# Optimization experiments

Hardware: AMD Instinct MI355X
Metric: run time of the kernel (lower is better)

## Reference

```python
import jax, jax.numpy as jnp
import numpy as np

B, T, H, E, L, C = 32, 512, 512, 256, 64, 128  # batch, seq, hidden, chan_emb, latent, num_channels
IN = E + H + L  # recurrent_input_size


def setup_inputs() -> dict:
    key = jax.random.key(0)
    ks = jax.random.split(key, 8)
    marks = jax.random.randint(ks[0], (B, T), 0, C)
    # strictly increasing event times per sequence
    timestamps = jnp.cumsum(jax.random.uniform(ks[1], (B, T)), axis=1)
    latent_state = jax.random.normal(ks[2], (B, L), dtype=jnp.float32)
    emb_table = jax.random.normal(ks[3], (C, E), dtype=jnp.float32) * 0.02
    W_cell = jax.random.normal(ks[4], (IN, 7 * H), dtype=jnp.float32) * (1.0 / np.sqrt(IN))
    b_cell = jnp.zeros((7 * H,), dtype=jnp.float32)
    W_init = jax.random.normal(ks[5], (L, 6 * H), dtype=jnp.float32) * (1.0 / np.sqrt(L))
    b_init = jnp.zeros((6 * H,), dtype=jnp.float32)
    return dict(marks=marks, timestamps=timestamps, latent_state=latent_state,
                emb_table=emb_table, W_cell=W_cell, b_cell=b_cell,
                W_init=W_init, b_init=b_init)


def reference(marks, timestamps, latent_state, emb_table, W_cell, b_cell, W_init, b_init):
    # time_embedding(timestamps): inter-event durations, [B, T, 1]
    time_deltas = jnp.concatenate(
        [timestamps[:, :1], timestamps[:, 1:] - timestamps[:, :-1]], axis=1)[..., None]
    emb = emb_table[marks]                                        # [B, T, E]
    lat = jnp.broadcast_to(latent_state[:, None, :], (B, T, L))   # [B, T, L]
    recurrent_input = jnp.concatenate([emb, lat], axis=-1)        # [B, T, E+L]

    # get_init_states via init_hidden_state_network
    init = latent_state @ W_init + b_init                         # [B, 6H]
    h_d0, c_d0, c_bar0, c0, delta0, o0 = jnp.split(init, 6, axis=-1)
    h_d0, c_d0, c_bar0, c0 = (jnp.tanh(h_d0), jnp.tanh(c_d0), jnp.tanh(c_bar0), jnp.tanh(c0))
    delta0 = jax.nn.softplus(delta0)
    o0 = jax.nn.sigmoid(o0)
    state0 = jnp.concatenate([h_d0, o0, c_bar0, c0, delta0], axis=-1)  # [B, 5H]

    def step(carry, xs):
        h_d, c_d, c_bar = carry
        r, dt = xs                                   # [B, E+L], [B, 1]
        feed = jnp.concatenate([r, h_d], axis=1)     # [B, IN]
        gates = feed @ W_cell + b_cell               # [B, 7H]
        gi, gf, gz, go, gib, gfb, gd = jnp.split(gates, 7, axis=-1)
        gi, gf, go = jax.nn.sigmoid(gi), jax.nn.sigmoid(gf), jax.nn.sigmoid(go)
        gib, gfb = jax.nn.sigmoid(gib), jax.nn.sigmoid(gfb)
        gz = jnp.tanh(gz)
        gd = jax.nn.softplus(gd)
        c_t = gf * c_d + gi * gz                     # recurrence uses decayed c as c_{t-1}
        c_bar_t = gfb * c_bar + gib * gz
        c_d_t = c_bar_t + (c_t - c_bar_t) * jnp.exp(-gd * dt)
        h_d_t = go * jnp.tanh(c_d_t)
        out = jnp.concatenate([h_d_t, go, c_bar_t, c_t, gd], axis=-1)  # [B, 5H]
        return (h_d_t, c_d_t, c_bar_t), out

    xs = (jnp.moveaxis(recurrent_input, 1, 0), jnp.moveaxis(time_deltas, 1, 0))
    _, outs = jax.lax.scan(step, (h_d0, c_d0, c_bar0), xs)           # [T, B, 5H]
    hidden_states = jnp.concatenate([state0[:, None, :], jnp.moveaxis(outs, 0, 1)], axis=1)
    return hidden_states  # [B, T+1, 5H]
```

## Files before the change

kernel.cpp:

```cpp
#include <hip/hip_runtime.h>
#include <hip/hip_bf16.h>

namespace {

constexpr int kB = 32;
constexpr int kT = 512;
constexpr int kH = 512;
constexpr int kE = 256;
constexpr int kL = 64;
constexpr int kNC = 7 * kH;
constexpr int kOutRow = 5 * kH;
constexpr int kBH = kB * kH;

typedef float f32x4 __attribute__((ext_vector_type(4)));
typedef short s16x8 __attribute__((ext_vector_type(8)));
typedef __bf16 bf16x8 __attribute__((ext_vector_type(8)));
typedef unsigned int u32x4 __attribute__((ext_vector_type(4)));
typedef unsigned int u32x2 __attribute__((ext_vector_type(2)));

__device__ __forceinline__ unsigned short f2bf(float f) {
  __hip_bfloat16 h = __float2bfloat16(f);
  return __builtin_bit_cast(unsigned short, h);
}

__device__ __forceinline__ float bf2f(unsigned short u) {
  return __builtin_bit_cast(float, (unsigned int)u << 16);
}

__device__ __forceinline__ float sigmoid_f(float x) {
  return 1.0f / (1.0f + expf(-x));
}
__device__ __forceinline__ float softplus_f(float x) {
  return fmaxf(x, 0.0f) + log1pf(expf(-fabsf(x)));
}

constexpr float kLog2e = 1.4426950408889634f;
constexpr float kLn2 = 0.6931471805599453f;
__device__ __forceinline__ float fexp2(float x) {
  return __builtin_amdgcn_exp2f(x);
}
__device__ __forceinline__ float frcp(float x) {
  return __builtin_amdgcn_rcpf(x);
}
__device__ __forceinline__ float fsigmoid(float x) {
  return frcp(1.0f + fexp2(-x * kLog2e));
}
__device__ __forceinline__ float ftanh(float x) {
  return 1.0f - 2.0f * frcp(1.0f + fexp2((2.0f * kLog2e) * x));
}
__device__ __forceinline__ float fsoftplus(float x) {
  return fmaxf(x, 0.0f) +
         kLn2 * __builtin_amdgcn_logf(1.0f + fexp2(-fabsf(x) * kLog2e));
}

__device__ __forceinline__ f32x4 mfma_bf16(s16x8 a, s16x8 b, f32x4 c) {
  return __builtin_amdgcn_mfma_f32_16x16x32_bf16(
      __builtin_bit_cast(bf16x8, a), __builtin_bit_cast(bf16x8, b), c, 0, 0, 0);
}

__device__ __forceinline__ void st_coh_x2(unsigned int* p, u32x2 v) {
  asm volatile("global_store_dwordx2 %0, %1, off sc0 sc1" :: "v"(p), "v"(v)
               : "memory");
}

__device__ __forceinline__ void unpack(const u32x4& x0, const u32x4& x1,
                                       s16x8& hi, s16x8& lo) {
#pragma unroll
  for (int e = 0; e < 4; ++e) {
    hi[e] = (short)(x0[e] & 0xffffu);
    hi[e + 4] = (short)(x1[e] & 0xffffu);
    lo[e] = (short)(x0[e] >> 16);
    lo[e + 4] = (short)(x1[e] >> 16);
  }
}

__global__ void hawkes_setup(const float* __restrict__ ts,
                             const float* __restrict__ latent,
                             const float* __restrict__ emb,
                             const float* __restrict__ Wc,
                             const float* __restrict__ bc,
                             const float* __restrict__ Wi,
                             const float* __restrict__ bi,
                             float* __restrict__ out,
                             float* __restrict__ emb_part,
                             float* __restrict__ lat_part,
                             float* __restrict__ dt,
                             float* __restrict__ cd0,
                             float* __restrict__ cb0,
                             unsigned int* __restrict__ hdtag) {
  const int blk = blockIdx.x;
  const int tid = threadIdx.x;
  if (blk < 112) {
    __shared__ float es[16][kE];
    const int cgrp = blk / 14;
    const int col = (blk % 14) * 256 + tid;
    for (int i = tid; i < 16 * kE; i += 256)
      es[i / kE][i % kE] = emb[(cgrp * 16 + i / kE) * kE + (i % kE)];
    __syncthreads();
    float acc[16];
#pragma unroll
    for (int c = 0; c < 16; ++c) acc[c] = 0.0f;
    for (int e = 0; e < kE; ++e) {
      const float w = Wc[(size_t)e * kNC + col];
#pragma unroll
      for (int c = 0; c < 16; ++c) acc[c] = fmaf(es[c][e], w, acc[c]);
    }
#pragma unroll
    for (int c = 0; c < 16; ++c)
      emb_part[(size_t)(cgrp * 16 + c) * kNC + col] = acc[c];
  } else if (blk < 126) {
    __shared__ float ls[kB][kL];
    const int col = (blk - 112) * 256 + tid;
    for (int i = tid; i < kB * kL; i += 256) ls[i / kL][i % kL] = latent[i];
    __syncthreads();
    float acc[kB];
    const float bias = bc[col];
#pragma unroll
    for (int b = 0; b < kB; ++b) acc[b] = bias;
    for (int l = 0; l < kL; ++l) {
      const float w = Wc[(size_t)(kE + l) * kNC + col];
#pragma unroll
      for (int b = 0; b < kB; ++b) acc[b] = fmaf(ls[b][l], w, acc[b]);
    }
#pragma unroll
    for (int b = 0; b < kB; ++b) lat_part[(size_t)b * kNC + col] = acc[b];
  } else if (blk < 222) {
    const int tg = (blk - 126) * 256 + tid;
    for (int it = 0; it < 4; ++it) {
      const int item = tg + it * 24576;
      const int b = item / 3072;
      const int c6 = item % 3072;
      float a = bi[c6];
      for (int l = 0; l < kL; ++l)
        a = fmaf(latent[b * kL + l], Wi[(size_t)l * 3072 + c6], a);
      const int which = c6 >> 9;
      const int jl = c6 & 511;
      float* orow = out + (size_t)b * (kT + 1) * kOutRow;
      if (which == 0) {
        const float h = tanhf(a);
        orow[jl] = h;
        const unsigned int hh = f2bf(h);
        const unsigned int hl = f2bf(h - bf2f((unsigned short)hh));
        u32x2 v0 = {hh | (hl << 16), 0u};
        u32x2 v1 = {0u, 0xFFFFFFFFu};
        st_coh_x2(hdtag + (size_t)(b * kH + jl) * 2, v0);
        st_coh_x2(hdtag + (size_t)(kBH + b * kH + jl) * 2, v1);
      } else if (which == 1) {
        cd0[b * kH + jl] = tanhf(a);
      } else if (which == 2) {
        const float v = tanhf(a);
        orow[2 * kH + jl] = v;
        cb0[b * kH + jl] = v;
      } else if (which == 3) {
        orow[3 * kH + jl] = tanhf(a);
      } else if (which == 4) {
        orow[4 * kH + jl] = softplus_f(a);
      } else {
        orow[kH + jl] = sigmoid_f(a);
      }
    }
  } else {
    const int idx = (blk - 222) * 256 + tid;
    const int b = idx >> 9;
    const int t = idx & 511;
    dt[idx] = (t == 0) ? ts[b * kT] : ts[b * kT + t] - ts[b * kT + t - 1];
  }
}

__global__ __launch_bounds__(512, 2) void hawkes_seq(
    const int* __restrict__ marks, const float* __restrict__ Wc,
    float* __restrict__ out, const float* __restrict__ emb_part,
    const float* __restrict__ lat_part, const float* __restrict__ dt,
    const float* __restrict__ cd0, const float* __restrict__ cb0,
    unsigned int* __restrict__ hdtag) {
  const int blk = blockIdx.x;
  const int bg = blk >> 5;
  const int jt = blk & 31;
  const int tid = threadIdx.x;
  const int wave = tid >> 6;
  const int lane = tid & 63;
  const int nl = lane & 15;
  const int kg = lane >> 4;

  __shared__ __align__(16) unsigned int lds_a[4][516];
  __shared__ float pl[8][7][16][4];

  s16x8 whi[7][2], wlo[7][2];
  {
    const float* Wh = Wc + (size_t)(kE + kL) * kNC;
    const int colbase = jt * 16 + nl;
#pragma unroll
    for (int g = 0; g < 7; ++g) {
#pragma unroll
      for (int kt = 0; kt < 2; ++kt) {
        s16x8 hi, lo;
#pragma unroll
        for (int e = 0; e < 8; ++e) {
          const float w =
              Wh[(size_t)(wave * 64 + kt * 32 + kg * 8 + e) * kNC +
                 g * kH + colbase];
          const unsigned short h = f2bf(w);
          hi[e] = (short)h;
          lo[e] = (short)f2bf(w - bf2f(h));
        }
        whi[g][kt] = hi;
        wlo[g][kt] = lo;
      }
    }
  }

  const int t4 = tid * 4;
  const int b_ld = t4 >> 9;
  const int k_ld = t4 & 511;
  unsigned int* ld_base =
      hdtag + (size_t)((bg * 4 + b_ld) * kH + k_ld) * 2;

  const int bl = lane >> 4;
  const int b_pw = bg * 4 + bl;
  const int j_pw = jt * 16 + nl;
  float c_d = 0.0f, c_bar = 0.0f, dtv = 0.0f;
  float rb[7];
#pragma unroll
  for (int m = 0; m < 7; ++m) rb[m] = 0.0f;
  if (wave == 0) {
    c_d = cd0[b_pw * kH + j_pw];
    c_bar = cb0[b_pw * kH + j_pw];
    const int mk = marks[b_pw * kT + 0];
    dtv = dt[b_pw * kT + 0];
#pragma unroll
    for (int m = 0; m < 7; ++m)
      rb[m] = emb_part[(size_t)mk * kNC + m * kH + j_pw] +
              lat_part[(size_t)b_pw * kNC + m * kH + j_pw];
  }

  for (int s = 1; s <= kT; ++s) {
    const unsigned int tg = (unsigned int)(s - 1);
    unsigned int* lp = ld_base + (size_t)((s - 1) & 1) * (kBH * 2);
    u32x4 d0, d1;
    for (;;) {
      asm volatile(
          "global_load_dwordx4 %0, %2, off sc0 sc1\n\t"
          "global_load_dwordx4 %1, %2, off offset:16 sc0 sc1\n\t"
          "s_waitcnt vmcnt(0)"
          : "=v"(d0), "=v"(d1) : "v"(lp) : "memory");
      if (d0[1] == tg && d0[3] == tg && d1[1] == tg && d1[3] == tg) break;
    }
    {
      u32x4 w = {d0[0], d0[2], d1[0], d1[2]};
      *(u32x4*)&lds_a[b_ld][k_ld] = w;
    }
    __syncthreads();

    const unsigned int* ap = &lds_a[nl & 3][wave * 64 + kg * 8];
    u32x4 x0 = *(const u32x4*)(ap);
    u32x4 x1 = *(const u32x4*)(ap + 4);
    u32x4 x2 = *(const u32x4*)(ap + 32);
    u32x4 x3 = *(const u32x4*)(ap + 36);
    s16x8 ah0, al0, ah1, al1;
    unpack(x0, x1, ah0, al0);
    unpack(x2, x3, ah1, al1);

    f32x4 acc[7];
#pragma unroll
    for (int g = 0; g < 7; ++g) {
      f32x4 a = {0.0f, 0.0f, 0.0f, 0.0f};
      a = mfma_bf16(ah0, whi[g][0], a);
      a = mfma_bf16(ah0, wlo[g][0], a);
      a = mfma_bf16(al0, whi[g][0], a);
      a = mfma_bf16(ah1, whi[g][1], a);
      a = mfma_bf16(ah1, wlo[g][1], a);
      a = mfma_bf16(al1, whi[g][1], a);
      acc[g] = a;
    }
    if (lane < 16) {
#pragma unroll
      for (int g = 0; g < 7; ++g)
        *(f32x4*)&pl[wave][g][nl][0] = acc[g];
    }
    __syncthreads();

    if (wave == 0) {
      float g[7];
#pragma unroll
      for (int m = 0; m < 7; ++m) {
        float a = rb[m];
#pragma unroll
        for (int w = 0; w < 8; ++w) a += pl[w][m][nl][bl];
        g[m] = a;
      }
      const float gi = fsigmoid(g[0]);
      const float gf = fsigmoid(g[1]);
      const float gz = ftanh(g[2]);
      const float go = fsigmoid(g[3]);
      const float gib = fsigmoid(g[4]);
      const float gfb = fsigmoid(g[5]);
      const float gd = fsoftplus(g[6]);

      const float c = fmaf(gf, c_d, gi * gz);
      c_bar = fmaf(gfb, c_bar, gib * gz);
      c_d = c_bar + (c - c_bar) * fexp2(-gd * dtv * kLog2e);
      const float hd = go * ftanh(c_d);

      const unsigned int hh = f2bf(hd);
      const unsigned int hl = f2bf(hd - bf2f((unsigned short)hh));
      u32x2 pub = {hh | (hl << 16), (unsigned int)s};
      st_coh_x2(hdtag + (size_t)((s & 1) * kBH + b_pw * kH + j_pw) * 2, pub);

      float* orow = out + ((size_t)b_pw * (kT + 1) + s) * kOutRow;
      __builtin_nontemporal_store(hd, orow + j_pw);
      __builtin_nontemporal_store(go, orow + kH + j_pw);
      __builtin_nontemporal_store(c_bar, orow + 2 * kH + j_pw);
      __builtin_nontemporal_store(c, orow + 3 * kH + j_pw);
      __builtin_nontemporal_store(gd, orow + 4 * kH + j_pw);

      if (s < kT) {
        const int mk = marks[b_pw * kT + s];
        dtv = dt[b_pw * kT + s];
#pragma unroll
        for (int m = 0; m < 7; ++m)
          rb[m] = emb_part[(size_t)mk * kNC + m * kH + j_pw] +
                  lat_part[(size_t)b_pw * kNC + m * kH + j_pw];
      }
    }
  }
}

}

extern "C" void kernel_launch(void* const* d_in, const int* in_sizes, int n_in,
                              void* d_out, int out_size, void* d_ws,
                              size_t ws_size, hipStream_t stream) {
  const int* marks = (const int*)d_in[0];
  const float* ts = (const float*)d_in[1];
  const float* latent = (const float*)d_in[2];
  const float* emb = (const float*)d_in[3];
  const float* Wc = (const float*)d_in[4];
  const float* bc = (const float*)d_in[5];
  const float* Wi = (const float*)d_in[6];
  const float* bi = (const float*)d_in[7];
  float* out = (float*)d_out;

  char* ws = (char*)d_ws;
  float* emb_part = (float*)(ws + 0);
  float* lat_part = (float*)(ws + 1835008);
  float* dt       = (float*)(ws + 2293760);
  float* cd0      = (float*)(ws + 2359296);
  float* cb0      = (float*)(ws + 2424832);
  unsigned int* hdtag = (unsigned int*)(ws + 2490368);

  hawkes_setup<<<286, 256, 0, stream>>>(ts, latent, emb, Wc, bc, Wi, bi, out,
                                        emb_part, lat_part, dt, cd0, cb0,
                                        hdtag);
  hawkes_seq<<<256, 512, 0, stream>>>(marks, Wc, out, emb_part, lat_part, dt,
                                      cd0, cb0, hdtag);
}
```

Measured before the change: 1.581 ms.

## Repartition recurrent kernel into 64 blocks of 16 batches each

The persistent recurrent kernel drops from 256 blocks of 512 threads (4 batches × 16 columns each) to 64 blocks of 256 threads (16 batches × 16 columns each). Each wave now covers 128 K rows, and all threads take part in the gate epilogue instead of only wave 0. The goal is fewer blocks polling the global h-state flags each step, more MFMA M-dimension use, and a shorter cross-wave reduction. In exchange each block does four times the work per step on a quarter of the blocks, and each thread issues 16 polling loads with higher register pressure.

```diff
diff --git a/kernel.cpp b/kernel.cpp
--- a/kernel.cpp
+++ b/kernel.cpp
@@ -167,14 +167,14 @@
   }
 }
 
-__global__ __launch_bounds__(512, 2) void hawkes_seq(
+__global__ __launch_bounds__(256, 1) void hawkes_seq(
     const int* __restrict__ marks, const float* __restrict__ Wc,
     float* __restrict__ out, const float* __restrict__ emb_part,
     const float* __restrict__ lat_part, const float* __restrict__ dt,
     const float* __restrict__ cd0, const float* __restrict__ cb0,
     unsigned int* __restrict__ hdtag) {
   const int blk = blockIdx.x;
-  const int bg = blk >> 5;
+  const int grp = blk >> 5;
   const int jt = blk & 31;
   const int tid = threadIdx.x;
   const int wave = tid >> 6;
@@ -182,22 +182,22 @@
   const int nl = lane & 15;
   const int kg = lane >> 4;
 
-  __shared__ __align__(16) unsigned int lds_a[4][516];
-  __shared__ float pl[8][7][16][4];
-
-  s16x8 whi[7][2], wlo[7][2];
+  __shared__ __align__(16) unsigned int lds_a[16][516];
+  __shared__ __align__(16) float pl[7][16][68];
+
+  s16x8 whi[7][4], wlo[7][4];
   {
     const float* Wh = Wc + (size_t)(kE + kL) * kNC;
     const int colbase = jt * 16 + nl;
 #pragma unroll
     for (int g = 0; g < 7; ++g) {
 #pragma unroll
-      for (int kt = 0; kt < 2; ++kt) {
+      for (int kt = 0; kt < 4; ++kt) {
         s16x8 hi, lo;
 #pragma unroll
         for (int e = 0; e < 8; ++e) {
           const float w =
-              Wh[(size_t)(wave * 64 + kt * 32 + kg * 8 + e) * kNC +
+              Wh[(size_t)(wave * 128 + kt * 32 + kg * 8 + e) * kNC +
                  g * kH + colbase];
           const unsigned short h = f2bf(w);
           hi[e] = (short)h;
@@ -209,92 +209,118 @@
     }
   }
 
-  const int t4 = tid * 4;
-  const int b_ld = t4 >> 9;
-  const int k_ld = t4 & 511;
-  unsigned int* ld_base =
-      hdtag + (size_t)((bg * 4 + b_ld) * kH + k_ld) * 2;
-
-  const int bl = lane >> 4;
-  const int b_pw = bg * 4 + bl;
-  const int j_pw = jt * 16 + nl;
-  float c_d = 0.0f, c_bar = 0.0f, dtv = 0.0f;
+  const int b_loc = tid >> 4;
+  const int j_loc = tid & 15;
+  const int b_glob = grp * 16 + b_loc;
+  const int u_pw = jt * 16 + j_loc;
+  float c_d = cd0[b_glob * kH + u_pw];
+  float c_bar = cb0[b_glob * kH + u_pw];
+  float dtv = dt[b_glob * kT + 0];
   float rb[7];
-#pragma unroll
-  for (int m = 0; m < 7; ++m) rb[m] = 0.0f;
-  if (wave == 0) {
-    c_d = cd0[b_pw * kH + j_pw];
-    c_bar = cb0[b_pw * kH + j_pw];
-    const int mk = marks[b_pw * kT + 0];
-    dtv = dt[b_pw * kT + 0];
+  {
+    const int mk = marks[b_glob * kT + 0];
 #pragma unroll
     for (int m = 0; m < 7; ++m)
-      rb[m] = emb_part[(size_t)mk * kNC + m * kH + j_pw] +
-              lat_part[(size_t)b_pw * kNC + m * kH + j_pw];
-  }
+      rb[m] = emb_part[(size_t)mk * kNC + m * kH + u_pw] +
+              lat_part[(size_t)b_glob * kNC + m * kH + u_pw];
+  }
+
+  const size_t grp_byte = (size_t)grp * 16 * kH * 8;
 
   for (int s = 1; s <= kT; ++s) {
     const unsigned int tg = (unsigned int)(s - 1);
-    unsigned int* lp = ld_base + (size_t)((s - 1) & 1) * (kBH * 2);
-    u32x4 d0, d1;
+    const char* pb = (const char*)hdtag +
+                     (size_t)((s - 1) & 1) * (kBH * 8) + grp_byte +
+                     (size_t)tid * 16 + 4096;
+    u32x4 d0, d1, d2, d3, d4, d5, d6, d7, d8, d9, d10, d11, d12, d13, d14,
+        d15;
     for (;;) {
       asm volatile(
-          "global_load_dwordx4 %0, %2, off sc0 sc1\n\t"
-          "global_load_dwordx4 %1, %2, off offset:16 sc0 sc1\n\t"
+          "global_load_dwordx4 %0, %16, off offset:-4096 sc0 sc1\n\t"
+          "global_load_dwordx4 %1, %16, off sc0 sc1\n\t"
+          "global_load_dwordx4 %2, %17, off offset:-4096 sc0 sc1\n\t"
+          "global_load_dwordx4 %3, %17, off sc0 sc1\n\t"
+          "global_load_dwordx4 %4, %18, off offset:-4096 sc0 sc1\n\t"
+          "global_load_dwordx4 %5, %18, off sc0 sc1\n\t"
+          "global_load_dwordx4 %6, %19, off offset:-4096 sc0 sc1\n\t"
+          "global_load_dwordx4 %7, %19, off sc0 sc1\n\t"
+          "global_load_dwordx4 %8, %20, off offset:-4096 sc0 sc1\n\t"
+          "global_load_dwordx4 %9, %20, off sc0 sc1\n\t"
+          "global_load_dwordx4 %10, %21, off offset:-4096 sc0 sc1\n\t"
+          "global_load_dwordx4 %11, %21, off sc0 sc1\n\t"
+          "global_load_dwordx4 %12, %22, off offset:-4096 sc0 sc1\n\t"
+          "global_load_dwordx4 %13, %22, off sc0 sc1\n\t"
+          "global_load_dwordx4 %14, %23, off offset:-4096 sc0 sc1\n\t"
+          "global_load_dwordx4 %15, %23, off sc0 sc1\n\t"
           "s_waitcnt vmcnt(0)"
-          : "=v"(d0), "=v"(d1) : "v"(lp) : "memory");
-      if (d0[1] == tg && d0[3] == tg && d1[1] == tg && d1[3] == tg) break;
+          : "=v"(d0), "=v"(d1), "=v"(d2), "=v"(d3), "=v"(d4), "=v"(d5),
+            "=v"(d6), "=v"(d7), "=v"(d8), "=v"(d9), "=v"(d10), "=v"(d11),
+            "=v"(d12), "=v"(d13), "=v"(d14), "=v"(d15)
+          : "v"(pb), "v"(pb + 8192), "v"(pb + 16384), "v"(pb + 24576),
+            "v"(pb + 32768), "v"(pb + 40960), "v"(pb + 49152),
+            "v"(pb + 57344)
+          : "memory");
+      const unsigned bad =
+          (d0[1] ^ tg) | (d0[3] ^ tg) | (d1[1] ^ tg) | (d1[3] ^ tg) |
+          (d2[1] ^ tg) | (d2[3] ^ tg) | (d3[1] ^ tg) | (d3[3] ^ tg) |
+          (d4[1] ^ tg) | (d4[3] ^ tg) | (d5[1] ^ tg) | (d5[3] ^ tg) |
+          (d6[1] ^ tg) | (d6[3] ^ tg) | (d7[1] ^ tg) | (d7[3] ^ tg) |
+          (d8[1] ^ tg) | (d8[3] ^ tg) | (d9[1] ^ tg) | (d9[3] ^ tg) |
+          (d10[1] ^ tg) | (d10[3] ^ tg) | (d11[1] ^ tg) | (d11[3] ^ tg) |
+          (d12[1] ^ tg) | (d12[3] ^ tg) | (d13[1] ^ tg) | (d13[3] ^ tg) |
+          (d14[1] ^ tg) | (d14[3] ^ tg) | (d15[1] ^ tg) | (d15[3] ^ tg);
+      if (bad == 0) break;
     }
     {
-      u32x4 w = {d0[0], d0[2], d1[0], d1[2]};
-      *(u32x4*)&lds_a[b_ld][k_ld] = w;
+      const int u2 = 2 * tid;
+#define STW(J, D)                                  \
+  {                                                \
+    u32x2 w = {D[0], D[2]};                        \
+    *(u32x2*)&lds_a[J][u2] = w;                    \
+  }
+      STW(0, d0) STW(1, d1) STW(2, d2) STW(3, d3) STW(4, d4) STW(5, d5)
+      STW(6, d6) STW(7, d7) STW(8, d8) STW(9, d9) STW(10, d10) STW(11, d11)
+      STW(12, d12) STW(13, d13) STW(14, d14) STW(15, d15)
+#undef STW
     }
     __syncthreads();
 
-    const unsigned int* ap = &lds_a[nl & 3][wave * 64 + kg * 8];
-    u32x4 x0 = *(const u32x4*)(ap);
-    u32x4 x1 = *(const u32x4*)(ap + 4);
-    u32x4 x2 = *(const u32x4*)(ap + 32);
-    u32x4 x3 = *(const u32x4*)(ap + 36);
-    s16x8 ah0, al0, ah1, al1;
-    unpack(x0, x1, ah0, al0);
-    unpack(x2, x3, ah1, al1);
-
     f32x4 acc[7];
 #pragma unroll
-    for (int g = 0; g < 7; ++g) {
-      f32x4 a = {0.0f, 0.0f, 0.0f, 0.0f};
-      a = mfma_bf16(ah0, whi[g][0], a);
-      a = mfma_bf16(ah0, wlo[g][0], a);
-      a = mfma_bf16(al0, whi[g][0], a);
-      a = mfma_bf16(ah1, whi[g][1], a);
-      a = mfma_bf16(ah1, wlo[g][1], a);
-      a = mfma_bf16(al1, whi[g][1], a);
-      acc[g] = a;
-    }
-    if (lane < 16) {
-#pragma unroll
-      for (int g = 0; g < 7; ++g)
-        *(f32x4*)&pl[wave][g][nl][0] = acc[g];
-    }
+    for (int g = 0; g < 7; ++g) acc[g] = (f32x4){0.0f, 0.0f, 0.0f, 0.0f};
+    const unsigned int* ap = &lds_a[nl][wave * 128 + kg * 8];
+#pragma unroll
+    for (int kt = 0; kt < 4; ++kt) {
+      const u32x4 x0 = *(const u32x4*)(ap + kt * 32);
+      const u32x4 x1 = *(const u32x4*)(ap + kt * 32 + 4);
+      s16x8 ah, al;
+      unpack(x0, x1, ah, al);
+#pragma unroll
+      for (int g = 0; g < 7; ++g) {
+        acc[g] = mfma_bf16(al, whi[g][kt], acc[g]);
+        acc[g] = mfma_bf16(ah, wlo[g][kt], acc[g]);
+        acc[g] = mfma_bf16(ah, whi[g][kt], acc[g]);
+      }
+    }
+#pragma unroll
+    for (int g = 0; g < 7; ++g)
+      *(f32x4*)&pl[g][nl][wave * 16 + kg * 4] = acc[g];
     __syncthreads();
 
-    if (wave == 0) {
-      float g[7];
+    {
+      float gv[7];
 #pragma unroll
       for (int m = 0; m < 7; ++m) {
-        float a = rb[m];
-#pragma unroll
-        for (int w = 0; w < 8; ++w) a += pl[w][m][nl][bl];
-        g[m] = a;
-      }
-      const float gi = fsigmoid(g[0]);
-      const float gf = fsigmoid(g[1]);
-      const float gz = ftanh(g[2]);
-      const float go = fsigmoid(g[3]);
-      const float gib = fsigmoid(g[4]);
-      const float gfb = fsigmoid(g[5]);
-      const float gd = fsoftplus(g[6]);
+        const float* q = &pl[m][j_loc][b_loc];
+        gv[m] = ((q[0] + q[16]) + (q[32] + q[48])) + rb[m];
+      }
+      const float gi = fsigmoid(gv[0]);
+      const float gf = fsigmoid(gv[1]);
+      const float gz = ftanh(gv[2]);
+      const float go = fsigmoid(gv[3]);
+      const float gib = fsigmoid(gv[4]);
+      const float gfb = fsigmoid(gv[5]);
+      const float gd = fsoftplus(gv[6]);
 
       const float c = fmaf(gf, c_d, gi * gz);
       c_bar = fmaf(gfb, c_bar, gib * gz);
@@ -304,22 +330,23 @@
       const unsigned int hh = f2bf(hd);
       const unsigned int hl = f2bf(hd - bf2f((unsigned short)hh));
       u32x2 pub = {hh | (hl << 16), (unsigned int)s};
-      st_coh_x2(hdtag + (size_t)((s & 1) * kBH + b_pw * kH + j_pw) * 2, pub);
-
-      float* orow = out + ((size_t)b_pw * (kT + 1) + s) * kOutRow;
-      __builtin_nontemporal_store(hd, orow + j_pw);
-      __builtin_nontemporal_store(go, orow + kH + j_pw);
-      __builtin_nontemporal_store(c_bar, orow + 2 * kH + j_pw);
-      __builtin_nontemporal_store(c, orow + 3 * kH + j_pw);
-      __builtin_nontemporal_store(gd, orow + 4 * kH + j_pw);
+      st_coh_x2(hdtag + (size_t)((s & 1) * kBH + b_glob * kH + u_pw) * 2,
+                pub);
+
+      float* orow = out + ((size_t)b_glob * (kT + 1) + s) * kOutRow;
+      __builtin_nontemporal_store(hd, orow + u_pw);
+      __builtin_nontemporal_store(go, orow + kH + u_pw);
+      __builtin_nontemporal_store(c_bar, orow + 2 * kH + u_pw);
+      __builtin_nontemporal_store(c, orow + 3 * kH + u_pw);
+      __builtin_nontemporal_store(gd, orow + 4 * kH + u_pw);
 
       if (s < kT) {
-        const int mk = marks[b_pw * kT + s];
-        dtv = dt[b_pw * kT + s];
+        const int mk = marks[b_glob * kT + s];
+        dtv = dt[b_glob * kT + s];
 #pragma unroll
         for (int m = 0; m < 7; ++m)
-          rb[m] = emb_part[(size_t)mk * kNC + m * kH + j_pw] +
-                  lat_part[(size_t)b_pw * kNC + m * kH + j_pw];
+          rb[m] = emb_part[(size_t)mk * kNC + m * kH + u_pw] +
+                  lat_part[(size_t)b_glob * kNC + m * kH + u_pw];
       }
     }
   }
@@ -351,6 +378,6 @@
   hawkes_setup<<<286, 256, 0, stream>>>(ts, latent, emb, Wc, bc, Wi, bi, out,
                                         emb_part, lat_part, dt, cd0, cb0,
                                         hdtag);
-  hawkes_seq<<<256, 512, 0, stream>>>(marks, Wc, out, emb_part, lat_part, dt,
-                                      cd0, cb0, hdtag);
-}
+  hawkes_seq<<<64, 256, 0, stream>>>(marks, Wc, out, emb_part, lat_part, dt,
+                                     cd0, cb0, hdtag);
+}
```

Measured after the change: 1.904 ms. 1.2x slower.

## Poll per-block step flags and load MFMA fragments directly from global

Applied to the files above, without the earlier changes.

Adds a per-(batch group, column tile) step counter that each producer block writes after publishing its h slice, and consumers spin on these flags before reading. Each wave now loads its own A-fragment straight from the tagged global buffer instead of staging through LDS, which removes one __syncthreads per step. The partial-sum LDS buffer is double-buffered by step parity. The trade is extra flag traffic and an extra store per block per step, while the tag check on the data is kept as a fallback.

```diff
diff --git a/kernel.cpp b/kernel.cpp
--- a/kernel.cpp
+++ b/kernel.cpp
@@ -56,6 +56,18 @@
 __device__ __forceinline__ f32x4 mfma_bf16(s16x8 a, s16x8 b, f32x4 c) {
   return __builtin_amdgcn_mfma_f32_16x16x32_bf16(
       __builtin_bit_cast(bf16x8, a), __builtin_bit_cast(bf16x8, b), c, 0, 0, 0);
+}
+
+__device__ __forceinline__ int ldflag(const int* p) {
+  int v;
+  asm volatile("global_load_dword %0, %1, off sc0 sc1\n\ts_waitcnt vmcnt(0)"
+               : "=v"(v) : "v"(p) : "memory");
+  return v;
+}
+
+__device__ __forceinline__ void st_coh_u32(unsigned int* p, unsigned int v) {
+  asm volatile("global_store_dword %0, %1, off sc0 sc1" :: "v"(p), "v"(v)
+               : "memory");
 }
 
 __device__ __forceinline__ void st_coh_x2(unsigned int* p, u32x2 v) {
@@ -87,7 +99,8 @@
                              float* __restrict__ dt,
                              float* __restrict__ cd0,
                              float* __restrict__ cb0,
-                             unsigned int* __restrict__ hdtag) {
+                             unsigned int* __restrict__ hdtag,
+                             int* __restrict__ flags) {
   const int blk = blockIdx.x;
   const int tid = threadIdx.x;
   if (blk < 112) {
@@ -164,6 +177,7 @@
     const int b = idx >> 9;
     const int t = idx & 511;
     dt[idx] = (t == 0) ? ts[b * kT] : ts[b * kT + t] - ts[b * kT + t - 1];
+    if (blk == 222) st_coh_u32((unsigned int*)&flags[tid], 0u);
   }
 }
 
@@ -172,7 +186,7 @@
     float* __restrict__ out, const float* __restrict__ emb_part,
     const float* __restrict__ lat_part, const float* __restrict__ dt,
     const float* __restrict__ cd0, const float* __restrict__ cb0,
-    unsigned int* __restrict__ hdtag) {
+    unsigned int* __restrict__ hdtag, int* __restrict__ flags) {
   const int blk = blockIdx.x;
   const int bg = blk >> 5;
   const int jt = blk & 31;
@@ -182,8 +196,7 @@
   const int nl = lane & 15;
   const int kg = lane >> 4;
 
-  __shared__ __align__(16) unsigned int lds_a[4][516];
-  __shared__ float pl[8][7][16][4];
+  __shared__ float pl[2][8][7][16][4];
 
   s16x8 whi[7][2], wlo[7][2];
   {
@@ -209,12 +222,6 @@
     }
   }
 
-  const int t4 = tid * 4;
-  const int b_ld = t4 >> 9;
-  const int k_ld = t4 & 511;
-  unsigned int* ld_base =
-      hdtag + (size_t)((bg * 4 + b_ld) * kH + k_ld) * 2;
-
   const int bl = lane >> 4;
   const int b_pw = bg * 4 + bl;
   const int j_pw = jt * 16 + nl;
@@ -233,68 +240,91 @@
               lat_part[(size_t)b_pw * kNC + m * kH + j_pw];
   }
 
+  const int arow = bg * 4 + (nl & 3);
+  const int* fpoll = flags + bg * 32 + wave * 4 + (lane & 3);
+  const size_t frag_elem = (size_t)(arow * kH + wave * 64 + kg * 8);
+
   for (int s = 1; s <= kT; ++s) {
     const unsigned int tg = (unsigned int)(s - 1);
-    unsigned int* lp = ld_base + (size_t)((s - 1) & 1) * (kBH * 2);
-    u32x4 d0, d1;
+
+    if (s > 1) {
+      const int target = s - 1;
+      int v;
+      do {
+        v = ldflag(fpoll);
+      } while (!__all(v >= target));
+    }
+
+    const char* ab = (const char*)hdtag +
+                     ((size_t)((s - 1) & 1) * kBH + frag_elem) * 8;
+    u32x4 d0, d1, d2, d3, d4, d5, d6, d7;
     for (;;) {
       asm volatile(
-          "global_load_dwordx4 %0, %2, off sc0 sc1\n\t"
-          "global_load_dwordx4 %1, %2, off offset:16 sc0 sc1\n\t"
+          "global_load_dwordx4 %0, %8, off sc0 sc1\n\t"
+          "global_load_dwordx4 %1, %8, off offset:16 sc0 sc1\n\t"
+          "global_load_dwordx4 %2, %8, off offset:32 sc0 sc1\n\t"
+          "global_load_dwordx4 %3, %8, off offset:48 sc0 sc1\n\t"
+          "global_load_dwordx4 %4, %8, off offset:256 sc0 sc1\n\t"
+          "global_load_dwordx4 %5, %8, off offset:272 sc0 sc1\n\t"
+          "global_load_dwordx4 %6, %8, off offset:288 sc0 sc1\n\t"
+          "global_load_dwordx4 %7, %8, off offset:304 sc0 sc1\n\t"
           "s_waitcnt vmcnt(0)"
-          : "=v"(d0), "=v"(d1) : "v"(lp) : "memory");
-      if (d0[1] == tg && d0[3] == tg && d1[1] == tg && d1[3] == tg) break;
-    }
+          : "=&v"(d0), "=&v"(d1), "=&v"(d2), "=&v"(d3), "=&v"(d4),
+            "=&v"(d5), "=&v"(d6), "=&v"(d7)
+          : "v"(ab) : "memory");
+      const unsigned bad =
+          (d0[1] ^ tg) | (d0[3] ^ tg) | (d1[1] ^ tg) | (d1[3] ^ tg) |
+          (d2[1] ^ tg) | (d2[3] ^ tg) | (d3[1] ^ tg) | (d3[3] ^ tg) |
+          (d4[1] ^ tg) | (d4[3] ^ tg) | (d5[1] ^ tg) | (d5[3] ^ tg) |
+          (d6[1] ^ tg) | (d6[3] ^ tg) | (d7[1] ^ tg) | (d7[3] ^ tg);
+      if (__all(bad == 0)) break;
+    }
+    s16x8 ah0, al0, ah1, al1;
     {
-      u32x4 w = {d0[0], d0[2], d1[0], d1[2]};
-      *(u32x4*)&lds_a[b_ld][k_ld] = w;
-    }
-    __syncthreads();
-
-    const unsigned int* ap = &lds_a[nl & 3][wave * 64 + kg * 8];
-    u32x4 x0 = *(const u32x4*)(ap);
-    u32x4 x1 = *(const u32x4*)(ap + 4);
-    u32x4 x2 = *(const u32x4*)(ap + 32);
-    u32x4 x3 = *(const u32x4*)(ap + 36);
-    s16x8 ah0, al0, ah1, al1;
-    unpack(x0, x1, ah0, al0);
-    unpack(x2, x3, ah1, al1);
-
+      u32x4 w0 = {d0[0], d0[2], d1[0], d1[2]};
+      u32x4 w1 = {d2[0], d2[2], d3[0], d3[2]};
+      unpack(w0, w1, ah0, al0);
+      u32x4 w2 = {d4[0], d4[2], d5[0], d5[2]};
+      u32x4 w3 = {d6[0], d6[2], d7[0], d7[2]};
+      unpack(w2, w3, ah1, al1);
+    }
+
+    const int p = s & 1;
     f32x4 acc[7];
 #pragma unroll
     for (int g = 0; g < 7; ++g) {
       f32x4 a = {0.0f, 0.0f, 0.0f, 0.0f};
+      a = mfma_bf16(al0, whi[g][0], a);
+      a = mfma_bf16(ah0, wlo[g][0], a);
       a = mfma_bf16(ah0, whi[g][0], a);
-      a = mfma_bf16(ah0, wlo[g][0], a);
-      a = mfma_bf16(al0, whi[g][0], a);
+      a = mfma_bf16(al1, whi[g][1], a);
+      a = mfma_bf16(ah1, wlo[g][1], a);
       a = mfma_bf16(ah1, whi[g][1], a);
-      a = mfma_bf16(ah1, wlo[g][1], a);
-      a = mfma_bf16(al1, whi[g][1], a);
       acc[g] = a;
     }
     if (lane < 16) {
 #pragma unroll
       for (int g = 0; g < 7; ++g)
-        *(f32x4*)&pl[wave][g][nl][0] = acc[g];
+        *(f32x4*)&pl[p][wave][g][nl][0] = acc[g];
     }
     __syncthreads();
 
     if (wave == 0) {
-      float g[7];
+      float gv[7];
 #pragma unroll
       for (int m = 0; m < 7; ++m) {
         float a = rb[m];
 #pragma unroll
-        for (int w = 0; w < 8; ++w) a += pl[w][m][nl][bl];
-        g[m] = a;
+        for (int w = 0; w < 8; ++w) a += pl[p][w][m][nl][bl];
+        gv[m] = a;
       }
-      const float gi = fsigmoid(g[0]);
-      const float gf = fsigmoid(g[1]);
-      const float gz = ftanh(g[2]);
-      const float go = fsigmoid(g[3]);
-      const float gib = fsigmoid(g[4]);
-      const float gfb = fsigmoid(g[5]);
-      const float gd = fsoftplus(g[6]);
+      const float gi = fsigmoid(gv[0]);
+      const float gf = fsigmoid(gv[1]);
+      const float gz = ftanh(gv[2]);
+      const float go = fsigmoid(gv[3]);
+      const float gib = fsigmoid(gv[4]);
+      const float gfb = fsigmoid(gv[5]);
+      const float gd = fsoftplus(gv[6]);
 
       const float c = fmaf(gf, c_d, gi * gz);
       c_bar = fmaf(gfb, c_bar, gib * gz);
@@ -305,6 +335,8 @@
       const unsigned int hl = f2bf(hd - bf2f((unsigned short)hh));
       u32x2 pub = {hh | (hl << 16), (unsigned int)s};
       st_coh_x2(hdtag + (size_t)((s & 1) * kBH + b_pw * kH + j_pw) * 2, pub);
+      if (lane == 0)
+        st_coh_u32((unsigned int*)(flags + bg * 32 + jt), (unsigned int)s);
 
       float* orow = out + ((size_t)b_pw * (kT + 1) + s) * kOutRow;
       __builtin_nontemporal_store(hd, orow + j_pw);
@@ -347,10 +379,11 @@
   float* cd0      = (float*)(ws + 2359296);
   float* cb0      = (float*)(ws + 2424832);
   unsigned int* hdtag = (unsigned int*)(ws + 2490368);
+  int* flags      = (int*)(ws + 2752512);
 
   hawkes_setup<<<286, 256, 0, stream>>>(ts, latent, emb, Wc, bc, Wi, bi, out,
                                         emb_part, lat_part, dt, cd0, cb0,
-                                        hdtag);
+                                        hdtag, flags);
   hawkes_seq<<<256, 512, 0, stream>>>(marks, Wc, out, emb_part, lat_part, dt,
-                                      cd0, cb0, hdtag);
-}
+                                      cd0, cb0, hdtag, flags);
+}
```

After: 2.601 ms. 1.65x slower.

## Spread gate activations across waves and drop the pre-MFMA block barrier

Applied to the files above, without the earlier changes.

Each wave now loads the slice of the published hidden state that only it consumes, so the first __syncthreads per step becomes a wave-local LDS wait. After one barrier, the partial-sum reduction and the nonlinearity for the seven gates run on seven waves in parallel, and the embedding prefetch is split across those waves. A dedicated eighth wave reads the activated gates from LDS and does the cell update, cutting the serial per-step critical path that wave 0 used to carry alone. This adds a second barrier per step, drops the two-blocks-per-CU launch bound, reorders the MFMA accumulation, and adds a spin-loop iteration cap that could silently use stale data if a producer is slow.

```diff
diff --git a/kernel.cpp b/kernel.cpp
--- a/kernel.cpp
+++ b/kernel.cpp
@@ -61,6 +61,12 @@
 __device__ __forceinline__ void st_coh_x2(unsigned int* p, u32x2 v) {
   asm volatile("global_store_dwordx2 %0, %1, off sc0 sc1" :: "v"(p), "v"(v)
                : "memory");
+}
+
+__device__ __forceinline__ void barrier_lds() {
+  __builtin_amdgcn_sched_barrier(0);
+  asm volatile("s_waitcnt lgkmcnt(0)\n\ts_barrier" ::: "memory");
+  __builtin_amdgcn_sched_barrier(0);
 }
 
 __device__ __forceinline__ void unpack(const u32x4& x0, const u32x4& x1,
@@ -167,7 +173,7 @@
   }
 }
 
-__global__ __launch_bounds__(512, 2) void hawkes_seq(
+__global__ __launch_bounds__(512) void hawkes_seq(
     const int* __restrict__ marks, const float* __restrict__ Wc,
     float* __restrict__ out, const float* __restrict__ emb_part,
     const float* __restrict__ lat_part, const float* __restrict__ dt,
@@ -183,14 +189,15 @@
   const int kg = lane >> 4;
 
   __shared__ __align__(16) unsigned int lds_a[4][516];
-  __shared__ float pl[8][7][16][4];
+  __shared__ __align__(16) float pl[8][7][16][4];
+  __shared__ __align__(16) float act[7][16][4];
 
   s16x8 whi[7][2], wlo[7][2];
   {
     const float* Wh = Wc + (size_t)(kE + kL) * kNC;
     const int colbase = jt * 16 + nl;
 #pragma unroll
-    for (int g = 0; g < 7; ++g) {
+    for (int gg = 0; gg < 7; ++gg) {
 #pragma unroll
       for (int kt = 0; kt < 2; ++kt) {
         s16x8 hi, lo;
@@ -198,45 +205,41 @@
         for (int e = 0; e < 8; ++e) {
           const float w =
               Wh[(size_t)(wave * 64 + kt * 32 + kg * 8 + e) * kNC +
-                 g * kH + colbase];
+                 gg * kH + colbase];
           const unsigned short h = f2bf(w);
           hi[e] = (short)h;
           lo[e] = (short)f2bf(w - bf2f(h));
         }
-        whi[g][kt] = hi;
-        wlo[g][kt] = lo;
+        whi[gg][kt] = hi;
+        wlo[gg][kt] = lo;
       }
     }
   }
-
-  const int t4 = tid * 4;
-  const int b_ld = t4 >> 9;
-  const int k_ld = t4 & 511;
-  unsigned int* ld_base =
-      hdtag + (size_t)((bg * 4 + b_ld) * kH + k_ld) * 2;
 
   const int bl = lane >> 4;
   const int b_pw = bg * 4 + bl;
   const int j_pw = jt * 16 + nl;
-  float c_d = 0.0f, c_bar = 0.0f, dtv = 0.0f;
-  float rb[7];
-#pragma unroll
-  for (int m = 0; m < 7; ++m) rb[m] = 0.0f;
-  if (wave == 0) {
+
+  float c_d = 0.0f, c_bar = 0.0f, dtv = 0.0f, rb = 0.0f;
+  if (wave == 7) {
     c_d = cd0[b_pw * kH + j_pw];
     c_bar = cb0[b_pw * kH + j_pw];
+    dtv = dt[b_pw * kT + 0];
+  } else {
     const int mk = marks[b_pw * kT + 0];
-    dtv = dt[b_pw * kT + 0];
-#pragma unroll
-    for (int m = 0; m < 7; ++m)
-      rb[m] = emb_part[(size_t)mk * kNC + m * kH + j_pw] +
-              lat_part[(size_t)b_pw * kNC + m * kH + j_pw];
-  }
+    rb = emb_part[(size_t)mk * kNC + wave * kH + j_pw] +
+         lat_part[(size_t)b_pw * kNC + wave * kH + j_pw];
+  }
+
+  const int b_ld = lane >> 4;
+  const int k_ld = wave * 64 + (lane & 15) * 4;
+  unsigned int* ld_base = hdtag + (size_t)((bg * 4 + b_ld) * kH + k_ld) * 2;
 
   for (int s = 1; s <= kT; ++s) {
     const unsigned int tg = (unsigned int)(s - 1);
     unsigned int* lp = ld_base + (size_t)((s - 1) & 1) * (kBH * 2);
     u32x4 d0, d1;
+    int guard = 0;
     for (;;) {
       asm volatile(
           "global_load_dwordx4 %0, %2, off sc0 sc1\n\t"
@@ -244,12 +247,15 @@
           "s_waitcnt vmcnt(0)"
           : "=v"(d0), "=v"(d1) : "v"(lp) : "memory");
       if (d0[1] == tg && d0[3] == tg && d1[1] == tg && d1[3] == tg) break;
+      if (++guard > (1 << 15)) break;
     }
     {
       u32x4 w = {d0[0], d0[2], d1[0], d1[2]};
       *(u32x4*)&lds_a[b_ld][k_ld] = w;
     }
-    __syncthreads();
+    __builtin_amdgcn_sched_barrier(0);
+    asm volatile("s_waitcnt lgkmcnt(0)" ::: "memory");
+    __builtin_amdgcn_sched_barrier(0);
 
     const unsigned int* ap = &lds_a[nl & 3][wave * 64 + kg * 8];
     u32x4 x0 = *(const u32x4*)(ap);
@@ -262,39 +268,48 @@
 
     f32x4 acc[7];
 #pragma unroll
-    for (int g = 0; g < 7; ++g) {
+    for (int gg = 0; gg < 7; ++gg) {
       f32x4 a = {0.0f, 0.0f, 0.0f, 0.0f};
-      a = mfma_bf16(ah0, whi[g][0], a);
-      a = mfma_bf16(ah0, wlo[g][0], a);
-      a = mfma_bf16(al0, whi[g][0], a);
-      a = mfma_bf16(ah1, whi[g][1], a);
-      a = mfma_bf16(ah1, wlo[g][1], a);
-      a = mfma_bf16(al1, whi[g][1], a);
-      acc[g] = a;
+      a = mfma_bf16(al0, whi[gg][0], a);
+      a = mfma_bf16(ah0, wlo[gg][0], a);
+      a = mfma_bf16(ah0, whi[gg][0], a);
+      a = mfma_bf16(al1, whi[gg][1], a);
+      a = mfma_bf16(ah1, wlo[gg][1], a);
+      a = mfma_bf16(ah1, whi[gg][1], a);
+      acc[gg] = a;
     }
     if (lane < 16) {
 #pragma unroll
-      for (int g = 0; g < 7; ++g)
-        *(f32x4*)&pl[wave][g][nl][0] = acc[g];
-    }
-    __syncthreads();
-
-    if (wave == 0) {
-      float g[7];
-#pragma unroll
-      for (int m = 0; m < 7; ++m) {
-        float a = rb[m];
-#pragma unroll
-        for (int w = 0; w < 8; ++w) a += pl[w][m][nl][bl];
-        g[m] = a;
+      for (int gg = 0; gg < 7; ++gg)
+        *(f32x4*)&pl[wave][gg][lane][0] = acc[gg];
+    }
+    barrier_lds();
+
+    if (wave < 7) {
+      float a = rb;
+#pragma unroll
+      for (int w = 0; w < 8; ++w) a += pl[w][wave][nl][bl];
+      float v;
+      if (wave == 2) v = ftanh(a);
+      else if (wave == 6) v = fsoftplus(a);
+      else v = fsigmoid(a);
+      act[wave][nl][bl] = v;
+      if (s < kT) {
+        const int mk = marks[b_pw * kT + s];
+        rb = emb_part[(size_t)mk * kNC + wave * kH + j_pw] +
+             lat_part[(size_t)b_pw * kNC + wave * kH + j_pw];
       }
-      const float gi = fsigmoid(g[0]);
-      const float gf = fsigmoid(g[1]);
-      const float gz = ftanh(g[2]);
-      const float go = fsigmoid(g[3]);
-      const float gib = fsigmoid(g[4]);
-      const float gfb = fsigmoid(g[5]);
-      const float gd = fsoftplus(g[6]);
+    }
+    barrier_lds();
+
+    if (wave == 7) {
+      const float gi = act[0][nl][bl];
+      const float gf = act[1][nl][bl];
+      const float gz = act[2][nl][bl];
+      const float go = act[3][nl][bl];
+      const float gib = act[4][nl][bl];
+      const float gfb = act[5][nl][bl];
+      const float gd = act[6][nl][bl];
 
       const float c = fmaf(gf, c_d, gi * gz);
       c_bar = fmaf(gfb, c_bar, gib * gz);
@@ -313,14 +328,7 @@
       __builtin_nontemporal_store(c, orow + 3 * kH + j_pw);
       __builtin_nontemporal_store(gd, orow + 4 * kH + j_pw);
 
-      if (s < kT) {
-        const int mk = marks[b_pw * kT + s];
-        dtv = dt[b_pw * kT + s];
-#pragma unroll
-        for (int m = 0; m < 7; ++m)
-          rb[m] = emb_part[(size_t)mk * kNC + m * kH + j_pw] +
-                  lat_part[(size_t)b_pw * kNC + m * kH + j_pw];
-      }
+      if (s < kT) dtv = dt[b_pw * kT + s];
     }
   }
 }
```

Result: slower. 1.774 ms (+12.2%).
